# Performance work log

Measured on AMD Instinct MI355X. Metric: run time of the kernel, lower is better.

The kernel has to match this reference:

```python
import jax, jax.numpy as jnp
import numpy as np

B = 4096  # number of graphs per batch


def _mlp(x, Ws, bs):
    # Linear+ReLU for all but last layer, final Linear (gn.mlp_fn convention)
    for W, b in zip(Ws[:-1], bs[:-1]):
        x = jax.nn.relu(x @ W + b)
    return x @ Ws[-1] + bs[-1]


def _embedding(x, batch, aWs, abs_):
    # per-node scalar attention, then attention-weighted scatter_mean over graphs
    a_x = _mlp(x, aWs, abs_)                       # [N, 1]
    num = jax.ops.segment_sum(x * a_x, batch, num_segments=B)   # [B, f_x]
    cnt = jax.ops.segment_sum(jnp.ones((x.shape[0],), x.dtype), batch,
                              num_segments=B)                    # [B]
    return num / jnp.maximum(cnt, 1.0)[:, None]


def setup_inputs() -> dict:
    key = jax.random.key(0)
    ks = jax.random.split(key, 16)
    N, fx, fout = 1000000, 64, 64
    s = lambda fan: 1.0 / np.sqrt(fan)
    inp = {
        'x1': jax.random.normal(ks[0], (N, fx), jnp.float32),
        'batch1': jnp.sort(jax.random.randint(ks[1], (N,), 0, B)),
        'x2': jax.random.normal(ks[2], (N, fx), jnp.float32),
        'batch2': jnp.sort(jax.random.randint(ks[3], (N,), 0, B)),
        'aW1': jax.random.normal(ks[4], (fx, 64), jnp.float32) * s(fx),
        'ab1': jnp.zeros((64,), jnp.float32),
        'aW2': jax.random.normal(ks[5], (64, 64), jnp.float32) * s(64),
        'ab2': jnp.zeros((64,), jnp.float32),
        'aW3': jax.random.normal(ks[6], (64, 1), jnp.float32) * s(64),
        'ab3': jnp.zeros((1,), jnp.float32),
        'fW1': jax.random.normal(ks[7], (2 * fx, 64), jnp.float32) * s(2 * fx),
        'fb1': jnp.zeros((64,), jnp.float32),
        'fW2': jax.random.normal(ks[8], (64, 64), jnp.float32) * s(64),
        'fb2': jnp.zeros((64,), jnp.float32),
        'fW3': jax.random.normal(ks[9], (64, fout), jnp.float32) * s(64),
        'fb3': jnp.zeros((fout,), jnp.float32),
    }
    return inp


def reference(x1, batch1, x2, batch2, aW1, ab1, aW2, ab2, aW3, ab3,
              fW1, fb1, fW2, fb2, fW3, fb3):
    aWs, abs_ = (aW1, aW2, aW3), (ab1, ab2, ab3)
    u1 = _embedding(x1, batch1, aWs, abs_)   # [B, f_x]
    u2 = _embedding(x2, batch2, aWs, abs_)   # [B, f_x]
    u = jnp.concatenate([u1, u2], axis=1)    # [B, 2*f_x]
    return _mlp(u, (fW1, fW2, fW3), (fb1, fb2, fb3))  # [B, f_out]
```

## Files before the change

kernel.cpp:

```cpp
#include <hip/hip_runtime.h>


#define NGRAPHS 4096
constexpr int LDP = 68;
constexpr int LDU = 132;
constexpr int LDXS = 72;

typedef short bf16x8 __attribute__((ext_vector_type(8)));
typedef float f32x4 __attribute__((ext_vector_type(4)));

union BF8 { bf16x8 v; unsigned u[4]; };

__device__ __forceinline__ unsigned short f2bf(float f) {
    unsigned u = __float_as_uint(f);
    return (unsigned short)((u + 0x7FFFu + ((u >> 16) & 1u)) >> 16);
}

__device__ __forceinline__ unsigned cvt_pk_bf16(float lo, float hi) {
    unsigned r;
    asm("v_cvt_pk_bf16_f32 %0, %1, %2" : "=v"(r) : "v"(lo), "v"(hi));
    return r;
}

__device__ __forceinline__ float bflo(unsigned u) { return __uint_as_float(u << 16); }
__device__ __forceinline__ float bfhi(unsigned u) { return __uint_as_float(u & 0xffff0000u); }

__device__ __forceinline__ int lower_bound_i(const int* __restrict__ arr, int n, int v) {
    int lo = 0, hi = n;
    while (lo < hi) {
        int mid = (lo + hi) >> 1;
        if (arr[mid] < v) lo = mid + 1; else hi = mid;
    }
    return lo;
}

__global__ __launch_bounds__(256)
void prep_kernel(const float* __restrict__ W1, const float* __restrict__ W2,
                 unsigned short* __restrict__ w1p, unsigned short* __restrict__ w2t) {
    int e = blockIdx.x * 256 + threadIdx.x;
    int r = e >> 6, k = e & 63;
    int ct = r >> 4, kb = (r >> 2) & 3, reg = r & 3;
    int pi = 32 * (ct >> 1) + 8 * kb + 4 * (ct & 1) + reg;
    w1p[e] = f2bf(W1[k * 64 + pi]);
    w2t[e] = f2bf(W2[k * 64 + r]);
}

__global__ __launch_bounds__(256)
void attn_scatter_mfma(const float* __restrict__ x1, const int* __restrict__ batch1, int N1, int nblk1,
                       const float* __restrict__ x2, const int* __restrict__ batch2, int N2,
                       const unsigned short* __restrict__ w1p, const unsigned short* __restrict__ w2t,
                       const float* __restrict__ b1, const float* __restrict__ b2,
                       const float* __restrict__ W3, const float* __restrict__ b3,
                       float* __restrict__ num) {
    __shared__ alignas(16) unsigned short W1L[64 * LDXS];
    __shared__ alignas(16) unsigned short W2L[64 * LDXS];
    __shared__ alignas(16) float coefF[192];
    __shared__ alignas(16) unsigned short Xs[4][16 * LDXS];

    const float* x; const int* batch; int N, col_off, blk;
    if ((int)blockIdx.x < nblk1) { x = x1; batch = batch1; N = N1; col_off = 0;  blk = blockIdx.x; }
    else                         { x = x2; batch = batch2; N = N2; col_off = 64; blk = blockIdx.x - nblk1; }

    const int t = threadIdx.x;
    const int w = t >> 6, l = t & 63;
    const int jj = l & 15, kb = l >> 4;
    const int base = blk * 256 + w * 64;

    float4 xq0[4], xq1[4], xq2[4], xq3[4];
#pragma unroll
    for (int q = 0; q < 4; ++q) {
        const int row = base + q * 16 + jj;
        float4 a0, a1, a2, a3;
        a0 = a1 = a2 = a3 = make_float4(0.f, 0.f, 0.f, 0.f);
        if (row < N) {
            const float* xr = x + (size_t)row * 64;
            a0 = *(const float4*)&xr[kb * 8];
            a1 = *(const float4*)&xr[kb * 8 + 4];
            a2 = *(const float4*)&xr[32 + kb * 8];
            a3 = *(const float4*)&xr[32 + kb * 8 + 4];
        }
        xq0[q] = a0; xq1[q] = a1; xq2[q] = a2; xq3[q] = a3;
    }

    {
        const uint4* s1 = (const uint4*)w1p;
        const uint4* s2 = (const uint4*)w2t;
#pragma unroll
        for (int r = 0; r < 2; ++r) {
            int e4 = t + 256 * r;
            int row = e4 >> 3, c4 = e4 & 7;
            *(uint4*)((char*)W1L + row * 144 + c4 * 16) = s1[e4];
            *(uint4*)((char*)W2L + row * 144 + c4 * 16) = s2[e4];
        }
        if (t < 64)       coefF[t] = b1[t];
        else if (t < 128) coefF[t] = b2[t - 64];
        else if (t < 192) coefF[t] = W3[t - 128];
    }
    __syncthreads();

    const bool wave_valid = (base < N);
    const int nvalid = wave_valid ? min(64, N - base) : 0;

    const int gball = batch[min(base + l, N - 1)];
    const int gprev = __shfl_up(gball, 1);
    const unsigned long long bal = __ballot(l > 0 && gball != gprev);
    const bool slow = (bal != 0ull) || (nvalid < 64);

    const float b3v = b3[0];
    unsigned short* Xw = Xs[w];

    float ac0 = 0.f, ac1 = 0.f, ac2 = 0.f, ac3 = 0.f;
    float sacc = 0.f;
    int gcur = __shfl(gball, 0);

#pragma unroll
    for (int q = 0; q < 4; ++q) {
        const int nbase = base + q * 16;
        const float4 c0 = xq0[q], c1 = xq1[q], c2 = xq2[q], c3 = xq3[q];

        BF8 xb0, xb1;
        xb0.u[0] = cvt_pk_bf16(c0.x, c0.y); xb0.u[1] = cvt_pk_bf16(c0.z, c0.w);
        xb0.u[2] = cvt_pk_bf16(c1.x, c1.y); xb0.u[3] = cvt_pk_bf16(c1.z, c1.w);
        xb1.u[0] = cvt_pk_bf16(c2.x, c2.y); xb1.u[1] = cvt_pk_bf16(c2.z, c2.w);
        xb1.u[2] = cvt_pk_bf16(c3.x, c3.y); xb1.u[3] = cvt_pk_bf16(c3.z, c3.w);
        *(bf16x8*)&Xw[jj * LDXS + kb * 8]      = xb0.v;
        *(bf16x8*)&Xw[jj * LDXS + 32 + kb * 8] = xb1.v;

        unsigned ph[8];
#pragma unroll
        for (int ct = 0; ct < 4; ++ct) {
            const unsigned short* wr = &W1L[(ct * 16 + jj) * LDXS + kb * 8];
            const bf16x8 wf0 = *(const bf16x8*)wr;
            const bf16x8 wf1 = *(const bf16x8*)(wr + 32);
            f32x4 acc = *(const f32x4*)&coefF[32 * (ct >> 1) + 8 * kb + 4 * (ct & 1)];
            acc = __builtin_amdgcn_mfma_f32_16x16x32_bf16(wf0, xb0.v, acc, 0, 0, 0);
            acc = __builtin_amdgcn_mfma_f32_16x16x32_bf16(wf1, xb1.v, acc, 0, 0, 0);
            ph[2 * ct]     = cvt_pk_bf16(fmaxf(acc[0], 0.f), fmaxf(acc[1], 0.f));
            ph[2 * ct + 1] = cvt_pk_bf16(fmaxf(acc[2], 0.f), fmaxf(acc[3], 0.f));
        }
        BF8 bh0, bh1;
        bh0.u[0] = ph[0]; bh0.u[1] = ph[1]; bh0.u[2] = ph[2]; bh0.u[3] = ph[3];
        bh1.u[0] = ph[4]; bh1.u[1] = ph[5]; bh1.u[2] = ph[6]; bh1.u[3] = ph[7];

        float p = 0.f;
#pragma unroll
        for (int ct = 0; ct < 4; ++ct) {
            const unsigned short* wr = &W2L[(ct * 16 + jj) * LDXS + kb * 8];
            const bf16x8 wf0 = *(const bf16x8*)wr;
            const bf16x8 wf1 = *(const bf16x8*)(wr + 32);
            f32x4 acc = { 0.f, 0.f, 0.f, 0.f };
            acc = __builtin_amdgcn_mfma_f32_16x16x32_bf16(wf0, bh0.v, acc, 0, 0, 0);
            acc = __builtin_amdgcn_mfma_f32_16x16x32_bf16(wf1, bh1.v, acc, 0, 0, 0);
            const f32x4 b2v = *(const f32x4*)&coefF[64 + ct * 16 + 4 * kb];
            const f32x4 w3v = *(const f32x4*)&coefF[128 + ct * 16 + 4 * kb];
            p += fmaxf(acc[0] + b2v[0], 0.f) * w3v[0]
               + fmaxf(acc[1] + b2v[1], 0.f) * w3v[1]
               + fmaxf(acc[2] + b2v[2], 0.f) * w3v[2]
               + fmaxf(acc[3] + b2v[3], 0.f) * w3v[3];
        }
        p += __shfl_xor(p, 16);
        p += __shfl_xor(p, 32);
        const float a = p + b3v;

        if (!slow) {
#pragma unroll
            for (int j = 0; j < 4; ++j) {
                const int row = kb * 4 + j;
                const float aj = __shfl(a, row);
                const uint2 xr2 = *(const uint2*)&Xw[row * LDXS + jj * 4];
                ac0 += bflo(xr2.x) * aj;
                ac1 += bfhi(xr2.x) * aj;
                ac2 += bflo(xr2.y) * aj;
                ac3 += bfhi(xr2.y) * aj;
            }
        } else if (wave_valid) {
            const int lim = min(16, N - nbase);
#pragma unroll
            for (int i = 0; i < 16; ++i) {
                if (i < lim) {
                    const int g = __shfl(gball, q * 16 + i);
                    const float ai = __shfl(a, i);
                    if (g != gcur) {
                        atomicAdd(&num[(size_t)gcur * 128 + col_off + l], sacc);
                        sacc = 0.f;
                        gcur = g;
                    }
                    sacc += __uint_as_float(((unsigned)Xw[i * LDXS + l]) << 16) * ai;
                }
            }
        }
    }

    if (!slow) {
        ac0 += __shfl_xor(ac0, 16); ac1 += __shfl_xor(ac1, 16);
        ac2 += __shfl_xor(ac2, 16); ac3 += __shfl_xor(ac3, 16);
        ac0 += __shfl_xor(ac0, 32); ac1 += __shfl_xor(ac1, 32);
        ac2 += __shfl_xor(ac2, 32); ac3 += __shfl_xor(ac3, 32);
        if (kb == 0) {
            const int g = __shfl(gball, 0);
            float* dst = &num[(size_t)g * 128 + col_off + jj * 4];
            atomicAdd(dst + 0, ac0);
            atomicAdd(dst + 1, ac1);
            atomicAdd(dst + 2, ac2);
            atomicAdd(dst + 3, ac3);
        }
    } else if (wave_valid) {
        atomicAdd(&num[(size_t)gcur * 128 + col_off + l], sacc);
    }
}

template<int K, int LDAa, int LDBb>
__device__ __forceinline__ void tile_gemm(const float* __restrict__ As,
                                          const float* __restrict__ Bs,
                                          float acc[4][4], int n0, int j0) {
#pragma unroll 4
    for (int k0 = 0; k0 < K; k0 += 4) {
        float4 a[4], wv[4];
#pragma unroll
        for (int i = 0; i < 4; i++) a[i] = *(const float4*)&As[(n0 + i) * LDAa + k0];
#pragma unroll
        for (int kk = 0; kk < 4; kk++) wv[kk] = *(const float4*)&Bs[(k0 + kk) * LDBb + j0];
#pragma unroll
        for (int i = 0; i < 4; i++) {
            const float av0 = a[i].x, av1 = a[i].y, av2 = a[i].z, av3 = a[i].w;
            acc[i][0] += av0 * wv[0].x; acc[i][1] += av0 * wv[0].y; acc[i][2] += av0 * wv[0].z; acc[i][3] += av0 * wv[0].w;
            acc[i][0] += av1 * wv[1].x; acc[i][1] += av1 * wv[1].y; acc[i][2] += av1 * wv[1].z; acc[i][3] += av1 * wv[1].w;
            acc[i][0] += av2 * wv[2].x; acc[i][1] += av2 * wv[2].y; acc[i][2] += av2 * wv[2].z; acc[i][3] += av2 * wv[2].w;
            acc[i][0] += av3 * wv[3].x; acc[i][1] += av3 * wv[3].y; acc[i][2] += av3 * wv[3].z; acc[i][3] += av3 * wv[3].w;
        }
    }
}

__global__ __launch_bounds__(256)
void final_mlp_kernel(const float* __restrict__ num,
                      const int* __restrict__ batch1, int N1,
                      const int* __restrict__ batch2, int N2,
                      const float* __restrict__ W1, const float* __restrict__ b1,
                      const float* __restrict__ W2, const float* __restrict__ b2,
                      const float* __restrict__ W3, const float* __restrict__ b3,
                      float* __restrict__ out) {
    __shared__ float Us[64 * LDU];
    __shared__ float W1s[128 * LDP];
    __shared__ float W2s[64 * LDP];
    __shared__ float W3s[64 * LDP];
    __shared__ float Hs[64 * LDP];
    __shared__ float inv1[64], inv2[64];

    const int t = threadIdx.x;
    const int rowbase = blockIdx.x * 64;

    if (t < 64) {
        int g = rowbase + t;
        int c = lower_bound_i(batch1, N1, g + 1) - lower_bound_i(batch1, N1, g);
        inv1[t] = 1.0f / (float)max(c, 1);
    } else if (t < 128) {
        int g = rowbase + (t - 64);
        int c = lower_bound_i(batch2, N2, g + 1) - lower_bound_i(batch2, N2, g);
        inv2[t - 64] = 1.0f / (float)max(c, 1);
    }

    {
        const float4* W1v = (const float4*)W1;
#pragma unroll
        for (int r = 0; r < 8; r++) {
            int e4 = t + 256 * r;
            int e = e4 * 4;
            int k = e / 64, j = e % 64;
            *(float4*)&W1s[k * LDP + j] = W1v[e4];
        }
        const float4* W2v = (const float4*)W2;
        const float4* W3v = (const float4*)W3;
#pragma unroll
        for (int r = 0; r < 4; r++) {
            int e4 = t + 256 * r;
            int e = e4 * 4;
            int k = e / 64, j = e % 64;
            *(float4*)&W2s[k * LDP + j] = W2v[e4];
            *(float4*)&W3s[k * LDP + j] = W3v[e4];
        }
    }
    __syncthreads();

    {
        const float4* nv = (const float4*)(num + (size_t)rowbase * 128);
#pragma unroll
        for (int r = 0; r < 8; r++) {
            int e4 = t + 256 * r;
            int e = e4 * 4;
            int row = e / 128, col = e % 128;
            float4 v = nv[e4];
            float s = (col < 64) ? inv1[row] : inv2[row];
            v.x *= s; v.y *= s; v.z *= s; v.w *= s;
            *(float4*)&Us[row * LDU + col] = v;
        }
    }
    __syncthreads();

    const int fg = t & 15, ng = t >> 4;
    const int j0 = fg * 4, n0 = ng * 4;

    float acc[4][4];
#pragma unroll
    for (int i = 0; i < 4; i++) { acc[i][0] = 0.f; acc[i][1] = 0.f; acc[i][2] = 0.f; acc[i][3] = 0.f; }
    tile_gemm<128, LDU, LDP>(Us, W1s, acc, n0, j0);
    {
        float4 bb = *(const float4*)&b1[j0];
#pragma unroll
        for (int i = 0; i < 4; i++) {
            float4 hv;
            hv.x = fmaxf(acc[i][0] + bb.x, 0.f);
            hv.y = fmaxf(acc[i][1] + bb.y, 0.f);
            hv.z = fmaxf(acc[i][2] + bb.z, 0.f);
            hv.w = fmaxf(acc[i][3] + bb.w, 0.f);
            *(float4*)&Hs[(n0 + i) * LDP + j0] = hv;
        }
    }
    __syncthreads();

#pragma unroll
    for (int i = 0; i < 4; i++) { acc[i][0] = 0.f; acc[i][1] = 0.f; acc[i][2] = 0.f; acc[i][3] = 0.f; }
    tile_gemm<64, LDP, LDP>(Hs, W2s, acc, n0, j0);
    {
        float4 bb = *(const float4*)&b2[j0];
#pragma unroll
        for (int i = 0; i < 4; i++) {
            float4 hv;
            hv.x = fmaxf(acc[i][0] + bb.x, 0.f);
            hv.y = fmaxf(acc[i][1] + bb.y, 0.f);
            hv.z = fmaxf(acc[i][2] + bb.z, 0.f);
            hv.w = fmaxf(acc[i][3] + bb.w, 0.f);
            *(float4*)&Us[(n0 + i) * LDU + j0] = hv;
        }
    }
    __syncthreads();

#pragma unroll
    for (int i = 0; i < 4; i++) { acc[i][0] = 0.f; acc[i][1] = 0.f; acc[i][2] = 0.f; acc[i][3] = 0.f; }
    tile_gemm<64, LDU, LDP>(Us, W3s, acc, n0, j0);
    {
        float4 bb = *(const float4*)&b3[j0];
#pragma unroll
        for (int i = 0; i < 4; i++) {
            float4 ov;
            ov.x = acc[i][0] + bb.x;
            ov.y = acc[i][1] + bb.y;
            ov.z = acc[i][2] + bb.z;
            ov.w = acc[i][3] + bb.w;
            *(float4*)&out[(size_t)(rowbase + n0 + i) * 64 + j0] = ov;
        }
    }
}

extern "C" void kernel_launch(void* const* d_in, const int* in_sizes, int n_in,
                              void* d_out, int out_size, void* d_ws, size_t ws_size,
                              hipStream_t stream) {
    const float* x1     = (const float*)d_in[0];
    const int*   batch1 = (const int*)d_in[1];
    const float* x2     = (const float*)d_in[2];
    const int*   batch2 = (const int*)d_in[3];
    const float* aW1    = (const float*)d_in[4];
    const float* ab1    = (const float*)d_in[5];
    const float* aW2    = (const float*)d_in[6];
    const float* ab2    = (const float*)d_in[7];
    const float* aW3    = (const float*)d_in[8];
    const float* ab3    = (const float*)d_in[9];
    const float* fW1    = (const float*)d_in[10];
    const float* fb1    = (const float*)d_in[11];
    const float* fW2    = (const float*)d_in[12];
    const float* fb2    = (const float*)d_in[13];
    const float* fW3    = (const float*)d_in[14];
    const float* fb3    = (const float*)d_in[15];

    const int N1 = in_sizes[0] / 64;
    const int N2 = in_sizes[2] / 64;

    unsigned short* w1p = (unsigned short*)d_ws;
    unsigned short* w2t = w1p + 64 * 64;
    float* num = (float*)((char*)d_ws + 16384);

    prep_kernel<<<dim3(16), dim3(256), 0, stream>>>(aW1, aW2, w1p, w2t);
    hipMemsetAsync(num, 0, (size_t)NGRAPHS * 128 * sizeof(float), stream);

    const int nblk1 = (N1 + 255) / 256;
    const int nblk2 = (N2 + 255) / 256;
    attn_scatter_mfma<<<dim3(nblk1 + nblk2), dim3(256), 0, stream>>>(
        x1, batch1, N1, nblk1, x2, batch2, N2,
        w1p, w2t, ab1, ab2, aW3, ab3, num);
    final_mlp_kernel<<<dim3(NGRAPHS / 64), dim3(256), 0, stream>>>(
        num, batch1, N1, batch2, N2, fW1, fb1, fW2, fb2, fW3, fb3, (float*)d_out);
}
```

Before: 154.7 us.

## Load x rows coalesced per quarter-tile and weight with fp32 values

Global loads of x are changed from strided per-lane fragments, all prefetched up front, to fully coalesced float4 row loads issued inside each 16-row step. The MFMA operand is then read back from LDS after the bf16 store. The fast-path weighted sum now uses the fp32 register values instead of re-reading bf16 from LDS. The final atomics are spread across all 64 lanes instead of 16 lanes doing 4 each. This trades the up-front prefetch (latency hiding) for better coalescing and fewer registers, and it adds an LDS round trip before the MFMA.

```diff
diff --git a/kernel.cpp b/kernel.cpp
--- a/kernel.cpp
+++ b/kernel.cpp
@@ -64,23 +64,8 @@
     const int t = threadIdx.x;
     const int w = t >> 6, l = t & 63;
     const int jj = l & 15, kb = l >> 4;
+    const int rg = l >> 4, cg = l & 15;
     const int base = blk * 256 + w * 64;
-
-    float4 xq0[4], xq1[4], xq2[4], xq3[4];
-#pragma unroll
-    for (int q = 0; q < 4; ++q) {
-        const int row = base + q * 16 + jj;
-        float4 a0, a1, a2, a3;
-        a0 = a1 = a2 = a3 = make_float4(0.f, 0.f, 0.f, 0.f);
-        if (row < N) {
-            const float* xr = x + (size_t)row * 64;
-            a0 = *(const float4*)&xr[kb * 8];
-            a1 = *(const float4*)&xr[kb * 8 + 4];
-            a2 = *(const float4*)&xr[32 + kb * 8];
-            a3 = *(const float4*)&xr[32 + kb * 8 + 4];
-        }
-        xq0[q] = a0; xq1[q] = a1; xq2[q] = a2; xq3[q] = a3;
-    }
 
     {
         const uint4* s1 = (const uint4*)w1p;
@@ -116,15 +101,34 @@
 #pragma unroll
     for (int q = 0; q < 4; ++q) {
         const int nbase = base + q * 16;
-        const float4 c0 = xq0[q], c1 = xq1[q], c2 = xq2[q], c3 = xq3[q];
-
-        BF8 xb0, xb1;
-        xb0.u[0] = cvt_pk_bf16(c0.x, c0.y); xb0.u[1] = cvt_pk_bf16(c0.z, c0.w);
-        xb0.u[2] = cvt_pk_bf16(c1.x, c1.y); xb0.u[3] = cvt_pk_bf16(c1.z, c1.w);
-        xb1.u[0] = cvt_pk_bf16(c2.x, c2.y); xb1.u[1] = cvt_pk_bf16(c2.z, c2.w);
-        xb1.u[2] = cvt_pk_bf16(c3.x, c3.y); xb1.u[3] = cvt_pk_bf16(c3.z, c3.w);
-        *(bf16x8*)&Xw[jj * LDXS + kb * 8]      = xb0.v;
-        *(bf16x8*)&Xw[jj * LDXS + 32 + kb * 8] = xb1.v;
+
+        float4 cx0, cx1, cx2, cx3;
+        cx0 = cx1 = cx2 = cx3 = make_float4(0.f, 0.f, 0.f, 0.f);
+        {
+            const int r0 = nbase + rg;
+            if (r0 < N)      cx0 = *(const float4*)&x[(size_t)r0 * 64 + cg * 4];
+            const int r1 = nbase + 4 + rg;
+            if (r1 < N)      cx1 = *(const float4*)&x[(size_t)r1 * 64 + cg * 4];
+            const int r2 = nbase + 8 + rg;
+            if (r2 < N)      cx2 = *(const float4*)&x[(size_t)r2 * 64 + cg * 4];
+            const int r3 = nbase + 12 + rg;
+            if (r3 < N)      cx3 = *(const float4*)&x[(size_t)r3 * 64 + cg * 4];
+        }
+
+        {
+            uint2 u;
+            u.x = cvt_pk_bf16(cx0.x, cx0.y); u.y = cvt_pk_bf16(cx0.z, cx0.w);
+            *(uint2*)&Xw[(0 + rg) * LDXS + cg * 4] = u;
+            u.x = cvt_pk_bf16(cx1.x, cx1.y); u.y = cvt_pk_bf16(cx1.z, cx1.w);
+            *(uint2*)&Xw[(4 + rg) * LDXS + cg * 4] = u;
+            u.x = cvt_pk_bf16(cx2.x, cx2.y); u.y = cvt_pk_bf16(cx2.z, cx2.w);
+            *(uint2*)&Xw[(8 + rg) * LDXS + cg * 4] = u;
+            u.x = cvt_pk_bf16(cx3.x, cx3.y); u.y = cvt_pk_bf16(cx3.z, cx3.w);
+            *(uint2*)&Xw[(12 + rg) * LDXS + cg * 4] = u;
+        }
+
+        const bf16x8 xbl0 = *(const bf16x8*)&Xw[jj * LDXS + kb * 8];
+        const bf16x8 xbl1 = *(const bf16x8*)&Xw[jj * LDXS + 32 + kb * 8];
 
         unsigned ph[8];
 #pragma unroll
@@ -133,8 +137,8 @@
             const bf16x8 wf0 = *(const bf16x8*)wr;
             const bf16x8 wf1 = *(const bf16x8*)(wr + 32);
             f32x4 acc = *(const f32x4*)&coefF[32 * (ct >> 1) + 8 * kb + 4 * (ct & 1)];
-            acc = __builtin_amdgcn_mfma_f32_16x16x32_bf16(wf0, xb0.v, acc, 0, 0, 0);
-            acc = __builtin_amdgcn_mfma_f32_16x16x32_bf16(wf1, xb1.v, acc, 0, 0, 0);
+            acc = __builtin_amdgcn_mfma_f32_16x16x32_bf16(wf0, xbl0, acc, 0, 0, 0);
+            acc = __builtin_amdgcn_mfma_f32_16x16x32_bf16(wf1, xbl1, acc, 0, 0, 0);
             ph[2 * ct]     = cvt_pk_bf16(fmaxf(acc[0], 0.f), fmaxf(acc[1], 0.f));
             ph[2 * ct + 1] = cvt_pk_bf16(fmaxf(acc[2], 0.f), fmaxf(acc[3], 0.f));
         }
@@ -163,16 +167,14 @@
         const float a = p + b3v;
 
         if (!slow) {
-#pragma unroll
-            for (int j = 0; j < 4; ++j) {
-                const int row = kb * 4 + j;
-                const float aj = __shfl(a, row);
-                const uint2 xr2 = *(const uint2*)&Xw[row * LDXS + jj * 4];
-                ac0 += bflo(xr2.x) * aj;
-                ac1 += bfhi(xr2.x) * aj;
-                ac2 += bflo(xr2.y) * aj;
-                ac3 += bfhi(xr2.y) * aj;
-            }
+            const float a0 = __shfl(a, 0 + rg);
+            const float a1 = __shfl(a, 4 + rg);
+            const float a2 = __shfl(a, 8 + rg);
+            const float a3 = __shfl(a, 12 + rg);
+            ac0 += cx0.x * a0 + cx1.x * a1 + cx2.x * a2 + cx3.x * a3;
+            ac1 += cx0.y * a0 + cx1.y * a1 + cx2.y * a2 + cx3.y * a3;
+            ac2 += cx0.z * a0 + cx1.z * a1 + cx2.z * a2 + cx3.z * a3;
+            ac3 += cx0.w * a0 + cx1.w * a1 + cx2.w * a2 + cx3.w * a3;
         } else if (wave_valid) {
             const int lim = min(16, N - nbase);
 #pragma unroll
@@ -196,14 +198,13 @@
         ac2 += __shfl_xor(ac2, 16); ac3 += __shfl_xor(ac3, 16);
         ac0 += __shfl_xor(ac0, 32); ac1 += __shfl_xor(ac1, 32);
         ac2 += __shfl_xor(ac2, 32); ac3 += __shfl_xor(ac3, 32);
-        if (kb == 0) {
-            const int g = __shfl(gball, 0);
-            float* dst = &num[(size_t)g * 128 + col_off + jj * 4];
-            atomicAdd(dst + 0, ac0);
-            atomicAdd(dst + 1, ac1);
-            atomicAdd(dst + 2, ac2);
-            atomicAdd(dst + 3, ac3);
-        }
+        float v = ac0;
+        v = (rg == 1) ? ac1 : v;
+        v = (rg == 2) ? ac2 : v;
+        v = (rg == 3) ? ac3 : v;
+        const int f = 4 * cg + rg;
+        const int g = __shfl(gball, 0);
+        atomicAdd(&num[(size_t)g * 128 + col_off + f], v);
     } else if (wave_valid) {
         atomicAdd(&num[(size_t)gcur * 128 + col_off + l], sacc);
     }
```

New measurement: 156.0 us. Within noise of the previous version (+0.9%).
